# Kernel tuning notes

Hardware: AMD Instinct MI355X
Metric: run time of the kernel (lower is better)

The kernel has to match this reference:

```python
import jax, jax.numpy as jnp
import numpy as np

N, C_IN, T, V = 64, 64, 64, 25
C_OUT = 64
DK = DV = 16
NH = 8
DKH, DVH = DK // NH, DV // NH
KT = 9
EPS = 1e-5


def make_pe(channel, joint_num, time_len):
    # temporal positional encoding: position index = frame id, repeated per joint
    pos = np.repeat(np.arange(time_len), joint_num).astype(np.float32)[:, None]
    pe = np.zeros((time_len * joint_num, channel), np.float32)
    div = np.exp(np.arange(0, channel, 2).astype(np.float32) * -(np.log(10000.0) / channel))
    pe[:, 0::2] = np.sin(pos * div)
    pe[:, 1::2] = np.cos(pos * div)
    return jnp.asarray(pe.reshape(time_len, joint_num, channel).transpose(2, 0, 1)[None])  # (1,C,time,joint)


def setup_inputs():
    key = jax.random.key(0)
    ks = jax.random.split(key, 17)
    rn = lambda k, s, sc=0.05: jax.random.normal(k, s, jnp.float32) * sc
    return {
        'x': jax.random.normal(ks[0], (N, C_IN, T, V), jnp.float32),
        'pe': make_pe(C_IN, V, 64),
        'data_bn_g': 1.0 + rn(ks[1], (C_IN * V,)),
        'data_bn_b': rn(ks[2], (C_IN * V,)),
        'qkv_w': rn(ks[3], (3 * DK + DV, C_IN), 0.1),
        'qkv_b': rn(ks[4], (3 * DK + DV,)),
        'attn_w': rn(ks[5], (DV, DV), 0.1),
        'attn_b': rn(ks[6], (DV,)),
        'tcn_w': rn(ks[7], (C_OUT - DV, C_IN, KT, 1), 0.05),
        'tcn_b': rn(ks[8], (C_OUT - DV,)),
        'tcn_bn_g': 1.0 + rn(ks[9], (C_OUT - DV,)),
        'tcn_bn_b': rn(ks[10], (C_OUT - DV,)),
        'fc1_w': rn(ks[11], (C_OUT // 2, C_OUT), 0.1),
        'fc1_b': rn(ks[12], (C_OUT // 2,)),
        'fc2_w': rn(ks[13], (C_OUT, C_OUT // 2), 0.1),
        'fc2_b': rn(ks[14], (C_OUT,)),
        'bn_g': 1.0 + rn(ks[15], (C_OUT,)),
        'bn_b': rn(ks[16], (C_OUT,)),
    }


def _bn_eval(x, g, b, axis=1):
    # eval-mode BatchNorm with running_mean=0, running_var=1
    shape = [1] * x.ndim
    shape[axis] = -1
    scale = g / jnp.sqrt(1.0 + EPS)
    return x * scale.reshape(shape) + b.reshape(shape)


def _qkv_heads(x2d, qkv_w, qkv_b):
    # x2d: (B, C, T); 1x1 conv == channel matmul; split q/k/g/v, g is projected but unused
    qkv = jnp.einsum('oc,bct->bot', qkv_w, x2d) + qkv_b[None, :, None]
    q, k, _g, v = jnp.split(qkv, [DK, 2 * DK, 3 * DK], axis=1)
    B = x2d.shape[0]
    split = lambda z, ch: z.reshape(B, NH, ch // NH, -1)  # (B, Nh, chh, T)
    q = split(q, DK) * (DKH ** -0.5)
    return q, split(k, DK), split(v, DV)


def reference(x, pe, data_bn_g, data_bn_b, qkv_w, qkv_b, attn_w, attn_b,
              tcn_w, tcn_b, tcn_bn_g, tcn_bn_b, fc1_w, fc1_b, fc2_w, fc2_b, bn_g, bn_b):
    y = x + pe[:, :, :T]                                 # positional encoding (N,C,T,V)
    x_sum = x
    # data_bn over flattened (C*V) channels
    xb = x.transpose(0, 1, 3, 2).reshape(N, C_IN * V, T)
    xb = _bn_eval(xb, data_bn_g, data_bn_b)
    xn = xb.reshape(N, C_IN, V, T).transpose(0, 1, 3, 2)  # (N,C,T,V)
    # fold joints into batch: (N*V, C, T)
    xf = xn.transpose(0, 3, 1, 2).reshape(N * V, C_IN, T)
    yf = y.transpose(0, 3, 1, 2).reshape(N * V, C_IN, T)
    fq, fk, fv = _qkv_heads(xf, qkv_w, qkv_b)
    pq, pk, _ = _qkv_heads(yf, qkv_w, qkv_b)
    mu_q = fq.mean(-1, keepdims=True)                     # (B,H,dkh,1)
    fqc = fq - mu_q
    logits_pos = jnp.einsum('bhcs,bhct->bhst', pq, pk)    # (B,H,T,T)
    pairwise = jnp.einsum('bhcs,bhct->bhst', fqc, fk)     # (B,H,T,T)
    unary = jnp.einsum('bhcs,bhct->bhst', mu_q, fk)       # (B,H,1,T)
    weights = jnp.tanh(pairwise + logits_pos) + jnp.tanh(unary + logits_pos)
    ao = jnp.einsum('bhst,bhct->bhsc', weights, fv)       # (B,H,T,dvh)
    # (B,H,1,T,dvh) -> permute(0,1,4,2,3) -> combine heads -> (B, DV, T)
    ao = ao.transpose(0, 1, 3, 2).reshape(N * V, DV, T)
    ao = jnp.einsum('oc,bct->bot', attn_w, ao) + attn_b[None, :, None]
    ao = ao.reshape(N, V, DV, T).transpose(0, 2, 3, 1)    # (N, DV, T, V)
    # temporal conv branch (Unit2D: conv(k=9 temporal) + eval BN)
    tc = jax.lax.conv_general_dilated(x_sum, tcn_w, (1, 1), ((KT // 2, KT // 2), (0, 0)),
                                      dimension_numbers=('NCHW', 'OIHW', 'NCHW'))
    tc = tc + tcn_b[None, :, None, None]
    tc = _bn_eval(tc, tcn_bn_g, tcn_bn_b)
    result = jnp.concatenate([tc, ao], axis=1) + x_sum    # residual (down is None)
    # SE-style channel gating
    se = result.mean(axis=(2, 3))                         # (N, C_OUT)
    gate = jax.nn.sigmoid(jax.nn.relu(se @ fc1_w.T + fc1_b) @ fc2_w.T + fc2_b)
    result = result * gate[:, :, None, None] + result
    result = _bn_eval(result, bn_g, bn_b)
    return jax.nn.relu(result)
```

## Files before the change

kernel.cpp:

```cpp
#include <hip/hip_runtime.h>
#include <hip/hip_bf16.h>
#include <math.h>

#define TV_ 1600
#define SCALE_K 2.885390081777927f
#define RS2_ 0.70710678118654752f

typedef __attribute__((ext_vector_type(8))) short bf16x8;
typedef __attribute__((ext_vector_type(4))) float f32x4;
typedef __attribute__((ext_vector_type(2))) __fp16 h2f;

__device__ __forceinline__ float tanh_scaled(float y) {
    y = fminf(44.f, fmaxf(-44.f, y));
    float e = __builtin_amdgcn_exp2f(y);
    float r = __builtin_amdgcn_rcpf(e + 1.f);
    return __builtin_fmaf(e, r, -r);
}

__device__ __forceinline__ ushort f2bf(float f) {
    __hip_bfloat16 h = __float2bfloat16(f);
    return *(ushort*)&h;
}
__device__ __forceinline__ float bf2f(ushort u) {
    uint w = ((uint)u) << 16;
    return __uint_as_float(w);
}

__global__ __launch_bounds__(256) void t1_kernel(
    const float* __restrict__ x, const float* __restrict__ pe,
    const float* __restrict__ tcn_w, const float* __restrict__ tg,
    const float* __restrict__ qkv_w, const float* __restrict__ qkv_b,
    ushort* __restrict__ rt, float* __restrict__ Sp, float* __restrict__ Tt,
    ushort* __restrict__ wb, ushort* __restrict__ wq, float* __restrict__ qb,
    ushort* __restrict__ pet)
{
    const int tid = threadIdx.x;
    const int bx = blockIdx.x, by = blockIdx.y;

    if (bx == 25) {
        #pragma unroll 1
        for (int j = 0; j < 9; ++j) {
            int idx = by * 256 + tid + j * 16384;
            if (idx < 27648) {
                int oc = idx / 576, kk = idx - oc * 576;
                int kt = kk >> 6, ci = kk & 63;
                float a = tg[oc] * rsqrtf(1.f + 1e-5f);
                wb[idx] = f2bf(tcn_w[(oc * 64 + ci) * 9 + kt] * a);
            } else if (idx < 32768) {
                int i2 = idx - 27648;
                int r = i2 >> 6, c = i2 & 63;
                int src; float sc;
                if (r < 16)      { src = r;      sc = RS2_; }
                else if (r < 32) { src = r;      sc = SCALE_K; }
                else if (r < 48) { src = r + 16; sc = 1.f; }
                else if (r < 64) { src = r - 48; sc = RS2_; }
                else             { src = r - 48; sc = SCALE_K; }
                wq[i2] = f2bf(qkv_w[src * 64 + c] * sc);
            } else if (idx < 32848) {
                int r = idx - 32768;
                int src; float sc;
                if (r < 16)      { src = r;      sc = RS2_; }
                else if (r < 32) { src = r;      sc = SCALE_K; }
                else if (r < 48) { src = r + 16; sc = 1.f; }
                else if (r < 64) { src = r - 48; sc = RS2_; }
                else             { src = r - 48; sc = SCALE_K; }
                qb[r] = qkv_b[src] * sc;
            } else if (idx < 135248) {
                int i3 = idx - 32848;
                int ci = i3 / 1600, tv = i3 - ci * 1600;
                pet[tv * 64 + ci] = f2bf(pe[ci * 1600 + tv]);
            }
        }
        return;
    }
    if (bx == 26) {
        const int n = by;
        #pragma unroll
        for (int it = 0; it < 2; ++it) {
            int item = tid + it * 256;
            int ci = item >> 3, slot = item & 7;
            int t = (slot < 4) ? slot : (56 + slot);
            const float* xp = x + (n * 64 + ci) * TV_ + t * 25;
            float s = 0.f;
            #pragma unroll
            for (int v = 0; v < 25; ++v) s += xp[v];
            Tt[(n * 64 + ci) * 8 + slot] = s;
        }
        return;
    }

    __shared__ ushort smt[64 * 66];
    const int tv0 = bx * 64;
    const int n = by;
    const int tvl = tid & 63, cig = tid >> 6;
    const int tv = tv0 + tvl;

    float psum[16];
    #pragma unroll
    for (int k = 0; k < 16; ++k) psum[k] = 0.f;
    #pragma unroll
    for (int k = 0; k < 16; ++k) {
        int ci = k * 4 + cig;
        float xv = x[(n * 64 + ci) * TV_ + tv];
        smt[tvl * 66 + ci] = f2bf(xv);
        psum[k] += xv;
    }
    #pragma unroll
    for (int k = 0; k < 16; ++k) {
        float s = psum[k];
        #pragma unroll
        for (int off = 32; off >= 1; off >>= 1) s += __shfl_down(s, off, 64);
        if (tvl == 0) Sp[(n * 25 + bx) * 64 + k * 4 + cig] = s;
    }
    __syncthreads();

    #pragma unroll
    for (int j = 0; j < 8; ++j) {
        int chunk = tid + j * 256;
        int tvr = chunk >> 5, p = chunk & 31;
        uint val = *(const uint*)&smt[tvr * 66 + p * 2];
        *(uint*)&rt[(n * TV_ + tv0 + tvr) * 64 + p * 2] = val;
    }
}

__global__ __launch_bounds__(256, 5) void score_kernel(
    const ushort* __restrict__ rt, const ushort* __restrict__ pet,
    const float* __restrict__ dbg, const float* __restrict__ dbb,
    const ushort* __restrict__ wq, const float* __restrict__ qb,
    const float* __restrict__ attn_w, const float* __restrict__ attn_b,
    float* __restrict__ aoc, float* __restrict__ sep)
{
    __shared__ float sm[5312];
    ushort* smu = (ushort*)sm;
    const int MU_ = 1056, AO = 1120;
    const int FKP = 2400, PKP = 2976, FVP = 3552, PQP = 4128, FQP = 4704;

    const int b = blockIdx.x;
    const int l = b >> 3;
    const int n = (b & 7) * 8 + l / 25;
    const int v = l % 25;
    const int tid = threadIdx.x;

    const int lane = tid & 63, wave = tid >> 6;
    const int m16 = lane & 15, q = lane >> 4;

    {
        const int part = tid & 7;
        const int ci0 = part * 8;
        const float rs = rsqrtf(1.f + 1e-5f);
        float sc8[8], sh8[8];
        #pragma unroll
        for (int i = 0; i < 8; ++i) {
            sc8[i] = dbg[(ci0 + i) * 25 + v] * rs;
            sh8[i] = dbb[(ci0 + i) * 25 + v];
        }
        #pragma unroll
        for (int j = 0; j < 2; ++j) {
            int t = (tid + j * 256) >> 3;
            uint4 xr = *(const uint4*)&rt[(n * TV_ + t * 25 + v) * 64 + ci0];
            uint4 pr = *(const uint4*)&pet[(t * 25 + v) * 64 + ci0];
            const ushort* xu = (const ushort*)&xr;
            const ushort* pu = (const ushort*)&pr;
            ushort xs[8], ys[8];
            #pragma unroll
            for (int i = 0; i < 8; ++i) {
                float xf = bf2f(xu[i]);
                xs[i] = f2bf(xf * sc8[i] + sh8[i]);
                ys[i] = f2bf(xf + bf2f(pu[i]));
            }
            *(uint4*)&smu[t * 72 + ci0] = *(uint4*)xs;
            *(uint4*)&smu[4608 + t * 72 + ci0] = *(uint4*)ys;
        }
    }
    __syncthreads();

    f32x4 acc[5];
    #pragma unroll
    for (int mt = 0; mt < 5; ++mt) acc[mt] = (f32x4){0.f, 0.f, 0.f, 0.f};
    #pragma unroll
    for (int kt = 0; kt < 2; ++kt) {
        const int koff = kt * 32 + q * 8;
        bf16x8 bx = *(const bf16x8*)&smu[(wave * 16 + m16) * 72 + koff];
        bf16x8 by = *(const bf16x8*)&smu[4608 + (wave * 16 + m16) * 72 + koff];
        #pragma unroll
        for (int mt = 0; mt < 5; ++mt) {
            bf16x8 a = *(const bf16x8*)&wq[(mt * 16 + m16) * 64 + koff];
            acc[mt] = __builtin_amdgcn_mfma_f32_16x16x32_bf16(a, (mt < 3) ? bx : by, acc[mt], 0, 0, 0);
        }
    }
    __syncthreads();

    {
        const int t = wave * 16 + m16;
        #pragma unroll
        for (int r = 0; r < 4; ++r)
            sm[(q * 4 + r) * 66 + t] = acc[0][r] + qb[q * 4 + r];
        *(h2f*)&sm[FKP + t * 9 + 2 * q] =
            __builtin_amdgcn_cvt_pkrtz(acc[1][0] + qb[16 + q * 4], acc[1][1] + qb[16 + q * 4 + 1]);
        *(h2f*)&sm[FKP + t * 9 + 2 * q + 1] =
            __builtin_amdgcn_cvt_pkrtz(acc[1][2] + qb[16 + q * 4 + 2], acc[1][3] + qb[16 + q * 4 + 3]);
        *(h2f*)&sm[FVP + t * 9 + 2 * q] =
            __builtin_amdgcn_cvt_pkrtz(acc[2][0] + qb[32 + q * 4], acc[2][1] + qb[32 + q * 4 + 1]);
        *(h2f*)&sm[FVP + t * 9 + 2 * q + 1] =
            __builtin_amdgcn_cvt_pkrtz(acc[2][2] + qb[32 + q * 4 + 2], acc[2][3] + qb[32 + q * 4 + 3]);
        *(h2f*)&sm[PQP + t * 9 + 2 * q] =
            __builtin_amdgcn_cvt_pkrtz(acc[3][0] + qb[48 + q * 4], acc[3][1] + qb[48 + q * 4 + 1]);
        *(h2f*)&sm[PQP + t * 9 + 2 * q + 1] =
            __builtin_amdgcn_cvt_pkrtz(acc[3][2] + qb[48 + q * 4 + 2], acc[3][3] + qb[48 + q * 4 + 3]);
        *(h2f*)&sm[PKP + t * 9 + 2 * q] =
            __builtin_amdgcn_cvt_pkrtz(acc[4][0] + qb[64 + q * 4], acc[4][1] + qb[64 + q * 4 + 1]);
        *(h2f*)&sm[PKP + t * 9 + 2 * q + 1] =
            __builtin_amdgcn_cvt_pkrtz(acc[4][2] + qb[64 + q * 4 + 2], acc[4][3] + qb[64 + q * 4 + 3]);
    }
    __syncthreads();

    if (tid < 64) {
        int ch = tid & 15, qq = tid >> 4;
        float s = 0.f;
        #pragma unroll
        for (int t = 0; t < 16; ++t) s += sm[ch * 66 + qq * 16 + t];
        sm[MU_ + qq * 16 + ch] = s;
    }
    __syncthreads();
    if (tid < 16) {
        float mval = (sm[MU_ + tid] + sm[MU_ + 16 + tid] + sm[MU_ + 32 + tid] + sm[MU_ + 48 + tid]) * (1.f / 64.f);
        sm[MU_ + tid] = mval;
    }
    __syncthreads();

    #pragma unroll
    for (int e = 0; e < 2; ++e) {
        int idx = tid * 2 + e;
        int s = idx >> 3, h = idx & 7;
        float a = sm[(2 * h) * 66 + s] - sm[MU_ + 2 * h];
        float c = sm[(2 * h + 1) * 66 + s] - sm[MU_ + 2 * h + 1];
        *(h2f*)&sm[FQP + s * 9 + h] = __builtin_amdgcn_cvt_pkrtz(a, c);
    }
    __syncthreads();

    const int g3 = tid & 7, m3 = tid >> 3;
    #pragma unroll 1
    for (int h = 0; h < 8; ++h) {
        const float mu0 = sm[MU_ + 2 * h], mu1 = sm[MU_ + 2 * h + 1];
        float fq0c[2], fq1c[2], pq0[2], pq1[2];
        #pragma unroll
        for (int js = 0; js < 2; ++js) {
            int s = 2 * m3 + js;
            h2f fq2 = *(const h2f*)&sm[FQP + s * 9 + h];
            h2f pq2 = *(const h2f*)&sm[PQP + s * 9 + h];
            fq0c[js] = (float)fq2.x; fq1c[js] = (float)fq2.y;
            pq0[js] = (float)pq2.x;  pq1[js] = (float)pq2.y;
        }
        float ao00 = 0.f, ao01 = 0.f, ao10 = 0.f, ao11 = 0.f;
        #pragma unroll
        for (int ch = 0; ch < 2; ++ch) {
            float fk0[4], fk1[4], pk0[4], pk1[4], fv0[4], fv1[4], un[4];
            #pragma unroll
            for (int j = 0; j < 4; ++j) {
                int t = 8 * g3 + ch * 4 + j;
                h2f fk2 = *(const h2f*)&sm[FKP + t * 9 + h];
                h2f pk2 = *(const h2f*)&sm[PKP + t * 9 + h];
                h2f fv2 = *(const h2f*)&sm[FVP + t * 9 + h];
                fk0[j] = (float)fk2.x; fk1[j] = (float)fk2.y;
                pk0[j] = (float)pk2.x; pk1[j] = (float)pk2.y;
                fv0[j] = (float)fv2.x; fv1[j] = (float)fv2.y;
                un[j] = mu0 * fk0[j] + mu1 * fk1[j];
            }
            #pragma unroll
            for (int js = 0; js < 2; ++js) {
                #pragma unroll
                for (int j = 0; j < 4; ++j) {
                    float lp = pq0[js] * pk0[j] + pq1[js] * pk1[j];
                    float a1 = fq0c[js] * fk0[j] + fq1c[js] * fk1[j] + lp;
                    float a2 = un[j] + lp;
                    float w = tanh_scaled(a1) + tanh_scaled(a2);
                    if (js == 0) { ao00 += w * fv0[j]; ao01 += w * fv1[j]; }
                    else         { ao10 += w * fv0[j]; ao11 += w * fv1[j]; }
                }
            }
        }
        #pragma unroll
        for (int off = 1; off <= 4; off <<= 1) {
            ao00 += __shfl_xor(ao00, off);
            ao01 += __shfl_xor(ao01, off);
            ao10 += __shfl_xor(ao10, off);
            ao11 += __shfl_xor(ao11, off);
        }
        if (g3 == 0) {
            sm[AO + (2 * m3) * 20 + 2 * h]         = ao00;
            sm[AO + (2 * m3) * 20 + 2 * h + 1]     = ao01;
            sm[AO + (2 * m3 + 1) * 20 + 2 * h]     = ao10;
            sm[AO + (2 * m3 + 1) * 20 + 2 * h + 1] = ao11;
        }
    }
    __syncthreads();

    const int t = tid & 63, oq = tid >> 6;
    float aorow[16];
    #pragma unroll
    for (int i = 0; i < 4; ++i)
        *(float4*)&aorow[i * 4] = *(const float4*)&sm[AO + t * 20 + i * 4];
    float* aop = aoc + (n * 25 + v) * 1024;
    #pragma unroll
    for (int j = 0; j < 4; ++j) {
        int o = oq * 4 + j;
        float acc4 = attn_b[o];
        #pragma unroll
        for (int c = 0; c < 16; ++c) acc4 += attn_w[o * 16 + c] * aorow[c];
        aop[o * 64 + t] = acc4;
        float ssum = acc4;
        #pragma unroll
        for (int off = 32; off >= 1; off >>= 1) ssum += __shfl_down(ssum, off, 64);
        if ((tid & 63) == 0) sep[(n * 25 + v) * 16 + o] = ssum;
    }
}

__global__ __launch_bounds__(512, 1) void tcn_mfma_kernel(
    const ushort* __restrict__ rt, const float* __restrict__ x,
    const ushort* __restrict__ wb,
    const float* __restrict__ tcn_b, const float* __restrict__ tg,
    const float* __restrict__ tb,
    const float* __restrict__ sep, const float* __restrict__ Sp,
    const float* __restrict__ Tt, const float* __restrict__ aoc,
    const float* __restrict__ fc1w, const float* __restrict__ fc1b,
    const float* __restrict__ fc2w, const float* __restrict__ fc2b,
    const float* __restrict__ bng, const float* __restrict__ bnb,
    float* __restrict__ out)
{
    __shared__ ushort xsl[600 * 72];
    __shared__ float U[576];
    __shared__ float gpart[432];
    __shared__ float SS[64], seL[64], hid[32], gateL[64];

    const int b = blockIdx.x;
    const int n = b >> 2, tile = b & 3;
    const int t0 = tile * 16;
    const int tid = threadIdx.x;
    const float rsbn = rsqrtf(1.f + 1e-5f);

    const int tvbase = (t0 - 4) * 25;
    for (int idx = tid; idx < 4800; idx += 512) {
        int r = idx >> 3, part = idx & 7;
        int tv = tvbase + r;
        uint4 val = make_uint4(0u, 0u, 0u, 0u);
        if (tv >= 0 && tv < TV_) val = *(const uint4*)&rt[(n * TV_ + tv) * 64 + part * 8];
        *(uint4*)&xsl[r * 72 + part * 8] = val;
    }

    if (tid < 64) {
        float S = 0.f;
        #pragma unroll 1
        for (int j = 0; j < 25; ++j) S += Sp[(n * 25 + j) * 64 + tid];
        SS[tid] = S;
        float T[8];
        #pragma unroll
        for (int j = 0; j < 8; ++j) T[j] = Tt[(n * 64 + tid) * 8 + j];
        U[tid * 9 + 0] = S - (T[4] + T[5] + T[6] + T[7]);
        U[tid * 9 + 1] = S - (T[5] + T[6] + T[7]);
        U[tid * 9 + 2] = S - (T[6] + T[7]);
        U[tid * 9 + 3] = S - T[7];
        U[tid * 9 + 4] = S;
        U[tid * 9 + 5] = S - T[0];
        U[tid * 9 + 6] = S - (T[0] + T[1]);
        U[tid * 9 + 7] = S - (T[0] + T[1] + T[2]);
        U[tid * 9 + 8] = S - (T[0] + T[1] + T[2] + T[3]);
    }
    __syncthreads();
    if (tid < 432) {
        int oc = tid / 9, kt = tid - oc * 9;
        float cs = 0.f;
        #pragma unroll
        for (int cb = 0; cb < 8; ++cb) {
            bf16x8 w8 = *(const bf16x8*)&wb[oc * 576 + kt * 64 + cb * 8];
            #pragma unroll
            for (int i = 0; i < 8; ++i)
                cs += bf2f((ushort)w8[i]) * U[(cb * 8 + i) * 9 + kt];
        }
        gpart[tid] = cs;
    }
    __syncthreads();
    if (tid < 64) {
        if (tid < 48) {
            float cs = 0.f;
            #pragma unroll
            for (int kt = 0; kt < 9; ++kt) cs += gpart[tid * 9 + kt];
            float a = tg[tid] * rsbn;
            float cb_ = tcn_b[tid] * a + tb[tid];
            seL[tid] = (a * cs + 1600.f * cb_ + SS[tid]) * (1.f / 1600.f);
        } else {
            float at = 0.f;
            #pragma unroll 1
            for (int j = 0; j < 25; ++j) at += sep[(n * 25 + j) * 16 + tid - 48];
            seL[tid] = (at + SS[tid]) * (1.f / 1600.f);
        }
    }
    __syncthreads();
    if (tid < 32) {
        float a = fc1b[tid];
        #pragma unroll
        for (int c = 0; c < 64; ++c) a += fc1w[tid * 64 + c] * seL[c];
        hid[tid] = fmaxf(a, 0.f);
    }
    __syncthreads();
    if (tid < 64) {
        float g = fc2b[tid];
        #pragma unroll
        for (int j = 0; j < 32; ++j) g += fc2w[tid * 32 + j] * hid[j];
        gateL[tid] = 1.f / (1.f + __expf(-g));
    }
    __syncthreads();

    const int lane = tid & 63, wave = tid >> 6;
    const int m16 = lane & 15, q = lane >> 4;
    const int nt0 = wave * 3;

    f32x4 acc[3][3];
    f32x4 acc24[3];
    #pragma unroll
    for (int i = 0; i < 3; ++i)
        #pragma unroll
        for (int mt = 0; mt < 3; ++mt)
            acc[i][mt] = (f32x4){0.f, 0.f, 0.f, 0.f};
    #pragma unroll
    for (int mt = 0; mt < 3; ++mt) acc24[mt] = (f32x4){0.f, 0.f, 0.f, 0.f};

    for (int ktile = 0; ktile < 18; ++ktile) {
        const int kt = ktile >> 1;
        const int cib = (ktile & 1) * 32 + q * 8;
        bf16x8 afr[3];
        #pragma unroll
        for (int mt = 0; mt < 3; ++mt)
            afr[mt] = *(const bf16x8*)&wb[(mt * 16 + m16) * 576 + ktile * 32 + q * 8];
        #pragma unroll
        for (int i = 0; i < 3; ++i) {
            int p = (nt0 + i) * 16 + m16;
            bf16x8 bfr = *(const bf16x8*)&xsl[(p + kt * 25) * 72 + cib];
            #pragma unroll
            for (int mt = 0; mt < 3; ++mt)
                acc[i][mt] = __builtin_amdgcn_mfma_f32_16x16x32_bf16(afr[mt], bfr, acc[i][mt], 0, 0, 0);
        }
        if (wave == 0) {
            int p = 24 * 16 + m16;
            bf16x8 bfr = *(const bf16x8*)&xsl[(p + kt * 25) * 72 + cib];
            #pragma unroll
            for (int mt = 0; mt < 3; ++mt)
                acc24[mt] = __builtin_amdgcn_mfma_f32_16x16x32_bf16(afr[mt], bfr, acc24[mt], 0, 0, 0);
        }
    }

    float cb3[3][4], m3_[3][4], bb3[3][4];
    #pragma unroll
    for (int mt = 0; mt < 3; ++mt)
        #pragma unroll
        for (int r = 0; r < 4; ++r) {
            int oc = mt * 16 + q * 4 + r;
            float a = tg[oc] * rsbn;
            cb3[mt][r] = tcn_b[oc] * a + tb[oc];
            m3_[mt][r] = (1.f + gateL[oc]) * (bng[oc] * rsbn);
            bb3[mt][r] = bnb[oc];
        }
    #pragma unroll
    for (int i = 0; i < 3; ++i) {
        int posg = tile * 400 + (nt0 + i) * 16 + m16;
        #pragma unroll
        for (int mt = 0; mt < 3; ++mt) {
            #pragma unroll
            for (int r = 0; r < 4; ++r) {
                int oc = mt * 16 + q * 4 + r;
                float val = acc[i][mt][r] + cb3[mt][r] + x[(n * 64 + oc) * TV_ + posg];
                out[(n * 64 + oc) * TV_ + posg] = fmaxf(val * m3_[mt][r] + bb3[mt][r], 0.f);
            }
        }
    }
    if (wave == 0) {
        int posg = tile * 400 + 24 * 16 + m16;
        #pragma unroll
        for (int mt = 0; mt < 3; ++mt) {
            #pragma unroll
            for (int r = 0; r < 4; ++r) {
                int oc = mt * 16 + q * 4 + r;
                float val = acc24[mt][r] + cb3[mt][r] + x[(n * 64 + oc) * TV_ + posg];
                out[(n * 64 + oc) * TV_ + posg] = fmaxf(val * m3_[mt][r] + bb3[mt][r], 0.f);
            }
        }
    }

    __syncthreads();
    float* ts = (float*)xsl;
    for (int task = tid; task < 1600; task += 512) {
        int v = task >> 6;
        int r = task & 63;
        int o = r >> 2, f = r & 3;
        float4 d = *(const float4*)&aoc[(n * 25 + v) * 1024 + o * 64 + tile * 16 + f * 4];
        float* dst = &ts[v * 257 + o * 16 + f * 4];
        dst[0] = d.x; dst[1] = d.y; dst[2] = d.z; dst[3] = d.w;
    }
    __syncthreads();
    for (int p4 = tid; p4 < 1600; p4 += 512) {
        int o = p4 / 100, r4 = p4 - o * 100;
        int base4 = (n * 64 + 48 + o) * 400 + tile * 100 + r4;
        float4 xr = ((const float4*)x)[base4];
        float4 val;
        #pragma unroll
        for (int e = 0; e < 4; ++e) {
            int pos = r4 * 4 + e;
            int lt = pos / 25, v = pos - lt * 25;
            ((float*)&val)[e] = ts[v * 257 + o * 16 + lt];
        }
        float mm = (1.f + gateL[48 + o]) * (bng[48 + o] * rsbn);
        float bb = bnb[48 + o];
        val.x = fmaxf((val.x + xr.x) * mm + bb, 0.f);
        val.y = fmaxf((val.y + xr.y) * mm + bb, 0.f);
        val.z = fmaxf((val.z + xr.z) * mm + bb, 0.f);
        val.w = fmaxf((val.w + xr.w) * mm + bb, 0.f);
        ((float4*)out)[base4] = val;
    }
}

extern "C" void kernel_launch(void* const* d_in, const int* in_sizes, int n_in,
                              void* d_out, int out_size, void* d_ws, size_t ws_size,
                              hipStream_t stream) {
    const float* x     = (const float*)d_in[0];
    const float* pe    = (const float*)d_in[1];
    const float* dbg   = (const float*)d_in[2];
    const float* dbb   = (const float*)d_in[3];
    const float* qkvw  = (const float*)d_in[4];
    const float* qkvb  = (const float*)d_in[5];
    const float* attnw = (const float*)d_in[6];
    const float* attnb = (const float*)d_in[7];
    const float* tcnw  = (const float*)d_in[8];
    const float* tcnb  = (const float*)d_in[9];
    const float* tcng  = (const float*)d_in[10];
    const float* tcnbb = (const float*)d_in[11];
    const float* fc1w  = (const float*)d_in[12];
    const float* fc1b  = (const float*)d_in[13];
    const float* fc2w  = (const float*)d_in[14];
    const float* fc2b  = (const float*)d_in[15];
    const float* bng   = (const float*)d_in[16];
    const float* bnb   = (const float*)d_in[17];

    float* out  = (float*)d_out;
    float* Sp   = (float*)d_ws;
    float* sep  = Sp + 102400;
    float* Tt   = sep + 25600;
    float* qb   = Tt + 32768;
    float* aoc  = qb + 96;
    ushort* wb  = (ushort*)(aoc + 1638400);
    ushort* wq  = wb + 27648;
    ushort* pet = wq + 5120;
    ushort* rt  = pet + 102400;

    t1_kernel<<<dim3(27, 64), dim3(256), 0, stream>>>(
        x, pe, tcnw, tcng, qkvw, qkvb, rt, Sp, Tt, wb, wq, qb, pet);
    score_kernel<<<dim3(1600), dim3(256), 0, stream>>>(rt, pet, dbg, dbb, wq, qb, attnw, attnb, aoc, sep);
    tcn_mfma_kernel<<<dim3(256), dim3(512), 0, stream>>>(
        rt, x, wb, tcnb, tcng, tcnbb, sep, Sp, Tt, aoc,
        fc1w, fc1b, fc2w, fc2b, bng, bnb, out);
}
```

Before: 208.0 us.

## Restructure attention LDS layout to head-major and use packed fp16 dot2

Moves the fp16 K/V/Q feature tiles in LDS from time-major (stride 9) to a head-major layout (stride 68). The inner attention loop can then fetch four time steps with one float4 load instead of many scalar loads. The two-term products are replaced with the packed fdot2 instruction, and the tanh helper drops its input clamp and uses a shorter 1-2r form. Intended effect is fewer LDS instructions and fewer VALU ops in the hot score loop. Removing the clamp risks inf/NaN handling for extreme inputs, but exp2 saturating to inf still gives r=0, so tanh stays finite.

```diff
diff --git a/kernel.cpp b/kernel.cpp
--- a/kernel.cpp
+++ b/kernel.cpp
@@ -10,11 +10,17 @@
 typedef __attribute__((ext_vector_type(4))) float f32x4;
 typedef __attribute__((ext_vector_type(2))) __fp16 h2f;
 
-__device__ __forceinline__ float tanh_scaled(float y) {
-    y = fminf(44.f, fmaxf(-44.f, y));
+union F4H { float4 f; h2f h[4]; };
+union F2H { float2 f; h2f h[2]; };
+
+__device__ __forceinline__ float tanh4(float y) {
     float e = __builtin_amdgcn_exp2f(y);
     float r = __builtin_amdgcn_rcpf(e + 1.f);
-    return __builtin_fmaf(e, r, -r);
+    return __builtin_fmaf(-2.f, r, 1.f);
+}
+
+__device__ __forceinline__ float dot2f(h2f a, h2f b, float c) {
+    return __builtin_amdgcn_fdot2(a, b, c, false);
 }
 
 __device__ __forceinline__ ushort f2bf(float f) {
@@ -132,8 +138,9 @@
 {
     __shared__ float sm[5312];
     ushort* smu = (ushort*)sm;
-    const int MU_ = 1056, AO = 1120;
-    const int FKP = 2400, PKP = 2976, FVP = 3552, PQP = 4128, FQP = 4704;
+    const int MU_ = 1056;
+    const int FK2 = 1120, PK2 = 1664, FV2 = 2208, PQ2 = 2752, FQ2 = 3296;
+    const int AO2 = 3840;
 
     const int b = blockIdx.x;
     const int l = b >> 3;
@@ -195,22 +202,15 @@
         #pragma unroll
         for (int r = 0; r < 4; ++r)
             sm[(q * 4 + r) * 66 + t] = acc[0][r] + qb[q * 4 + r];
-        *(h2f*)&sm[FKP + t * 9 + 2 * q] =
-            __builtin_amdgcn_cvt_pkrtz(acc[1][0] + qb[16 + q * 4], acc[1][1] + qb[16 + q * 4 + 1]);
-        *(h2f*)&sm[FKP + t * 9 + 2 * q + 1] =
-            __builtin_amdgcn_cvt_pkrtz(acc[1][2] + qb[16 + q * 4 + 2], acc[1][3] + qb[16 + q * 4 + 3]);
-        *(h2f*)&sm[FVP + t * 9 + 2 * q] =
-            __builtin_amdgcn_cvt_pkrtz(acc[2][0] + qb[32 + q * 4], acc[2][1] + qb[32 + q * 4 + 1]);
-        *(h2f*)&sm[FVP + t * 9 + 2 * q + 1] =
-            __builtin_amdgcn_cvt_pkrtz(acc[2][2] + qb[32 + q * 4 + 2], acc[2][3] + qb[32 + q * 4 + 3]);
-        *(h2f*)&sm[PQP + t * 9 + 2 * q] =
-            __builtin_amdgcn_cvt_pkrtz(acc[3][0] + qb[48 + q * 4], acc[3][1] + qb[48 + q * 4 + 1]);
-        *(h2f*)&sm[PQP + t * 9 + 2 * q + 1] =
-            __builtin_amdgcn_cvt_pkrtz(acc[3][2] + qb[48 + q * 4 + 2], acc[3][3] + qb[48 + q * 4 + 3]);
-        *(h2f*)&sm[PKP + t * 9 + 2 * q] =
-            __builtin_amdgcn_cvt_pkrtz(acc[4][0] + qb[64 + q * 4], acc[4][1] + qb[64 + q * 4 + 1]);
-        *(h2f*)&sm[PKP + t * 9 + 2 * q + 1] =
-            __builtin_amdgcn_cvt_pkrtz(acc[4][2] + qb[64 + q * 4 + 2], acc[4][3] + qb[64 + q * 4 + 3]);
+        const int p0 = (2 * q) * 68 + t, p1 = (2 * q + 1) * 68 + t;
+        *(h2f*)&sm[FK2 + p0] = __builtin_amdgcn_cvt_pkrtz(acc[1][0] + qb[16 + 4 * q],     acc[1][1] + qb[16 + 4 * q + 1]);
+        *(h2f*)&sm[FK2 + p1] = __builtin_amdgcn_cvt_pkrtz(acc[1][2] + qb[16 + 4 * q + 2], acc[1][3] + qb[16 + 4 * q + 3]);
+        *(h2f*)&sm[FV2 + p0] = __builtin_amdgcn_cvt_pkrtz(acc[2][0] + qb[32 + 4 * q],     acc[2][1] + qb[32 + 4 * q + 1]);
+        *(h2f*)&sm[FV2 + p1] = __builtin_amdgcn_cvt_pkrtz(acc[2][2] + qb[32 + 4 * q + 2], acc[2][3] + qb[32 + 4 * q + 3]);
+        *(h2f*)&sm[PQ2 + p0] = __builtin_amdgcn_cvt_pkrtz(acc[3][0] + qb[48 + 4 * q],     acc[3][1] + qb[48 + 4 * q + 1]);
+        *(h2f*)&sm[PQ2 + p1] = __builtin_amdgcn_cvt_pkrtz(acc[3][2] + qb[48 + 4 * q + 2], acc[3][3] + qb[48 + 4 * q + 3]);
+        *(h2f*)&sm[PK2 + p0] = __builtin_amdgcn_cvt_pkrtz(acc[4][0] + qb[64 + 4 * q],     acc[4][1] + qb[64 + 4 * q + 1]);
+        *(h2f*)&sm[PK2 + p1] = __builtin_amdgcn_cvt_pkrtz(acc[4][2] + qb[64 + 4 * q + 2], acc[4][3] + qb[64 + 4 * q + 3]);
     }
     __syncthreads();
 
@@ -234,48 +234,46 @@
         int s = idx >> 3, h = idx & 7;
         float a = sm[(2 * h) * 66 + s] - sm[MU_ + 2 * h];
         float c = sm[(2 * h + 1) * 66 + s] - sm[MU_ + 2 * h + 1];
-        *(h2f*)&sm[FQP + s * 9 + h] = __builtin_amdgcn_cvt_pkrtz(a, c);
+        *(h2f*)&sm[FQ2 + h * 68 + s] = __builtin_amdgcn_cvt_pkrtz(a, c);
     }
     __syncthreads();
 
     const int g3 = tid & 7, m3 = tid >> 3;
+    const int tb0 = 8 * g3;
     #pragma unroll 1
     for (int h = 0; h < 8; ++h) {
-        const float mu0 = sm[MU_ + 2 * h], mu1 = sm[MU_ + 2 * h + 1];
-        float fq0c[2], fq1c[2], pq0[2], pq1[2];
-        #pragma unroll
-        for (int js = 0; js < 2; ++js) {
-            int s = 2 * m3 + js;
-            h2f fq2 = *(const h2f*)&sm[FQP + s * 9 + h];
-            h2f pq2 = *(const h2f*)&sm[PQP + s * 9 + h];
-            fq0c[js] = (float)fq2.x; fq1c[js] = (float)fq2.y;
-            pq0[js] = (float)pq2.x;  pq1[js] = (float)pq2.y;
-        }
+        const int hb = h * 68;
+        h2f mupk = __builtin_amdgcn_cvt_pkrtz(sm[MU_ + 2 * h], sm[MU_ + 2 * h + 1]);
+        F2H fq2u, pq2u;
+        fq2u.f = *(const float2*)&sm[FQ2 + hb + 2 * m3];
+        pq2u.f = *(const float2*)&sm[PQ2 + hb + 2 * m3];
         float ao00 = 0.f, ao01 = 0.f, ao10 = 0.f, ao11 = 0.f;
         #pragma unroll
         for (int ch = 0; ch < 2; ++ch) {
-            float fk0[4], fk1[4], pk0[4], pk1[4], fv0[4], fv1[4], un[4];
+            const int base = hb + tb0 + 4 * ch;
+            F4H fk4, pk4, fv4;
+            fk4.f = *(const float4*)&sm[FK2 + base];
+            pk4.f = *(const float4*)&sm[PK2 + base];
+            fv4.f = *(const float4*)&sm[FV2 + base];
+            float un[4], fv0[4], fv1[4];
             #pragma unroll
             for (int j = 0; j < 4; ++j) {
-                int t = 8 * g3 + ch * 4 + j;
-                h2f fk2 = *(const h2f*)&sm[FKP + t * 9 + h];
-                h2f pk2 = *(const h2f*)&sm[PKP + t * 9 + h];
-                h2f fv2 = *(const h2f*)&sm[FVP + t * 9 + h];
-                fk0[j] = (float)fk2.x; fk1[j] = (float)fk2.y;
-                pk0[j] = (float)pk2.x; pk1[j] = (float)pk2.y;
-                fv0[j] = (float)fv2.x; fv1[j] = (float)fv2.y;
-                un[j] = mu0 * fk0[j] + mu1 * fk1[j];
+                un[j] = dot2f(mupk, fk4.h[j], 0.f);
+                fv0[j] = (float)fv4.h[j].x;
+                fv1[j] = (float)fv4.h[j].y;
             }
             #pragma unroll
             for (int js = 0; js < 2; ++js) {
+                h2f fq1 = fq2u.h[js];
+                h2f pq1 = pq2u.h[js];
                 #pragma unroll
                 for (int j = 0; j < 4; ++j) {
-                    float lp = pq0[js] * pk0[j] + pq1[js] * pk1[j];
-                    float a1 = fq0c[js] * fk0[j] + fq1c[js] * fk1[j] + lp;
+                    float lp = dot2f(pq1, pk4.h[j], 0.f);
+                    float a1 = dot2f(fq1, fk4.h[j], lp);
                     float a2 = un[j] + lp;
-                    float w = tanh_scaled(a1) + tanh_scaled(a2);
-                    if (js == 0) { ao00 += w * fv0[j]; ao01 += w * fv1[j]; }
-                    else         { ao10 += w * fv0[j]; ao11 += w * fv1[j]; }
+                    float w = tanh4(a1) + tanh4(a2);
+                    if (js == 0) { ao00 = __builtin_fmaf(w, fv0[j], ao00); ao01 = __builtin_fmaf(w, fv1[j], ao01); }
+                    else         { ao10 = __builtin_fmaf(w, fv0[j], ao10); ao11 = __builtin_fmaf(w, fv1[j], ao11); }
                 }
             }
         }
@@ -287,10 +285,10 @@
             ao11 += __shfl_xor(ao11, off);
         }
         if (g3 == 0) {
-            sm[AO + (2 * m3) * 20 + 2 * h]         = ao00;
-            sm[AO + (2 * m3) * 20 + 2 * h + 1]     = ao01;
-            sm[AO + (2 * m3 + 1) * 20 + 2 * h]     = ao10;
-            sm[AO + (2 * m3 + 1) * 20 + 2 * h + 1] = ao11;
+            sm[AO2 + (2 * m3) * 20 + 2 * h]         = ao00;
+            sm[AO2 + (2 * m3) * 20 + 2 * h + 1]     = ao01;
+            sm[AO2 + (2 * m3 + 1) * 20 + 2 * h]     = ao10;
+            sm[AO2 + (2 * m3 + 1) * 20 + 2 * h + 1] = ao11;
         }
     }
     __syncthreads();
@@ -299,7 +297,7 @@
     float aorow[16];
     #pragma unroll
     for (int i = 0; i < 4; ++i)
-        *(float4*)&aorow[i * 4] = *(const float4*)&sm[AO + t * 20 + i * 4];
+        *(float4*)&aorow[i * 4] = *(const float4*)&sm[AO2 + t * 20 + i * 4];
     float* aop = aoc + (n * 25 + v) * 1024;
     #pragma unroll
     for (int j = 0; j < 4; ++j) {
```

Result: faster. 202.2 us (-2.8%).
